# Kernel tuning notes

Measured on AMD Instinct MI355X. Metric: run time of the kernel, lower is better.

Reference implementation:

```python
import jax, jax.numpy as jnp
import numpy as np
from functools import partial

# CUBA LIF/LI constants (from init_kwargs / hxtorch CUBALIFParams defaults)
DT = 1e-6
TAU_MEM = 8e-6
TAU_SYN = 8e-6
DV = DT / TAU_MEM  # 0.125 membrane integration factor
DI = DT / TAU_SYN  # 0.125 synaptic decay factor
ALPHA = 50.0       # SuperSpike surrogate sharpness
THRESHOLD = 1.0    # spike threshold (leak = reset = 0)


@partial(jax.custom_vjp, nondiff_argnums=(1,))
def superspike(x, alpha):
    # Heaviside forward, SuperSpike surrogate backward
    return (x > 0.0).astype(x.dtype)

def _ss_fwd(x, alpha):
    return superspike(x, alpha), x

def _ss_bwd(alpha, x, g):
    return (g / (alpha * jnp.abs(x) + 1.0) ** 2,)

superspike.defvjp(_ss_fwd, _ss_bwd)


def setup_inputs() -> dict:
    key = jax.random.key(0)
    k1, k2, k3 = jax.random.split(key, 3)
    T, B, N_IN, N_H, N_OUT = 512, 128, 256, 1024, 32
    # Bernoulli(0.1) input spike trains (0/1 floats)
    spikes = (jax.random.uniform(k1, (T, B, N_IN)) < 0.1).astype(jnp.float32)
    w_h = jax.random.normal(k2, (N_H, N_IN), jnp.float32) * 0.1
    w_o = jax.random.normal(k3, (N_OUT, N_H), jnp.float32) * 0.05
    return {"spikes": spikes, "w_h": w_h, "w_o": w_o}


def _lif_scan(c):
    # c: [T, B, H] synaptic input currents; returns spike trace z: [T, B, H]
    B, H = c.shape[1], c.shape[2]
    def step(carry, c_t):
        v, i = carry
        i = i * (1.0 - DI) + c_t                 # synaptic current decay + input
        v = v + DV * (i - v)                      # membrane leaky integration (leak=0)
        z = superspike(v - THRESHOLD, ALPHA)      # spike
        zd = jax.lax.stop_gradient(z)
        v = (1.0 - zd) * v                        # reset to 0 (detached spike)
        return (v, i), z
    init = (jnp.zeros((B, H), c.dtype), jnp.zeros((B, H), c.dtype))
    _, z = jax.lax.scan(step, init, c)
    return z


def _li_scan(c):
    # c: [T, B, O]; returns membrane trace v: [T, B, O] (no spike/reset)
    B, O = c.shape[1], c.shape[2]
    def step(carry, c_t):
        v, i = carry
        i = i * (1.0 - DI) + c_t
        v = v + DV * (i - v)
        return (v, i), v
    init = (jnp.zeros((B, O), c.dtype), jnp.zeros((B, O), c.dtype))
    _, v = jax.lax.scan(step, init, c)
    return v


def reference(spikes, w_h, w_o):
    # hidden synapse: dense projection for all timesteps at once
    c_h = jnp.einsum('tbi,hi->tbh', spikes, w_h)
    # hidden CUBA LIF layer (sequential recurrence over time)
    z_h = _lif_scan(c_h)
    # output synapse
    c_o = jnp.einsum('tbh,oh->tbo', z_h, w_o)
    # readout CUBA LI layer -> membrane trace [T, B, n_out]
    return _li_scan(c_o)
```

## Files before the change

kernel.cpp:

```cpp
#include <hip/hip_runtime.h>
#include <stdint.h>

#define T_STEPS 512
#define BATCH   128
#define N_IN    256
#define N_H     1024
#define N_OUT   32

typedef __attribute__((ext_vector_type(2))) float f32x2;


__global__ __launch_bounds__(256) void k_prep(const float* __restrict__ spikes,
                                              uint32_t* __restrict__ pm,
                                              uint16_t* __restrict__ pt,
                                              uint32_t* __restrict__ cnts) {
    __shared__ uint16_t list[64];
    __shared__ uint32_t wcnt[4];
    const int tid = threadIdx.x;
    const int wave = tid >> 6, lane = tid & 63;
    for (int r = 0; r < 4; ++r) {
        const int row = blockIdx.x * 4 + r;
        float s = spikes[(size_t)row * N_IN + tid];
        bool act = s > 0.5f;
        unsigned long long m = __ballot(act);
        if (tid < 64) list[tid] = 256;
        if (lane == 0) wcnt[wave] = (uint32_t)__popcll(m);
        __syncthreads();
        uint32_t off = 0;
        for (int w = 0; w < wave; ++w) off += wcnt[w];
        uint32_t total = wcnt[0] + wcnt[1] + wcnt[2] + wcnt[3];
        if (act) {
            uint32_t pos = off + (uint32_t)__popcll(m & ((1ull << lane) - 1ull));
            if (pos < 64) list[pos] = (uint16_t)tid;
        }
        __syncthreads();
        if (tid < 32) {
            int h = tid >> 4, sl = tid & 15;
            pm[(uint32_t)row * 32 + tid] = ((uint32_t)list[2 * sl + h]) << 8;
        } else if (tid < 64) {
            int u = tid & 31;
            int h = u >> 4, sl = u & 15;
            pt[(uint32_t)row * 32 + u] = list[32 + 2 * sl + h];
        }
        if (tid == 0) cnts[row] = total < 64u ? total : 64u;
        __syncthreads();
    }
}

__global__ __launch_bounds__(256) void k_tr(const float* __restrict__ w_h,
                                            float* __restrict__ w_t) {
    int gid = blockIdx.x * 256 + threadIdx.x;
    int h = gid >> 8, i = gid & 255;
    w_t[(size_t)i * N_H + h] = w_h[gid];
}

__device__ __forceinline__ float xadd32(float x) {
    float a = x, b = x;
    asm("v_permlane32_swap_b32 %0, %1" : "+v"(a), "+v"(b));
    return a + b;
}

struct IdxSet { uint4 a, b, c, d; };

__global__ __launch_bounds__(256) void k_lif(const uint32_t* __restrict__ pm,
                                             const uint16_t* __restrict__ pt,
                                             const uint32_t* __restrict__ cnts,
                                             const float* __restrict__ w_t,
                                             uint32_t* __restrict__ zmask) {
    extern __shared__ __align__(16) float wl[];
    const int bg = blockIdx.x >> 4, tile = blockIdx.x & 15;
    const int h0 = tile * 64, tid = threadIdx.x;

    #pragma unroll 8
    for (int k = 0; k < 16; ++k) {
        int idx = (k << 8) + tid;
        int i = idx >> 4, c4 = (idx & 15) << 2;
        *(float4*)(wl + i * 64 + c4) =
            *(const float4*)(w_t + (size_t)i * N_H + h0 + c4);
    }
    if (tid < 64) wl[256 * 64 + tid] = 0.0f;
    __syncthreads();

    const int wv = __builtin_amdgcn_readfirstlane(tid >> 6);
    const int b  = (bg << 2) + wv;
    const int l  = tid & 63;
    const int duo2 = (l & 31) << 1;
    const int half16 = (l >> 5) << 4;
    const int half32 = (l >> 5) << 4;
    const char* wlb = (const char*)wl + (duo2 << 2);

    int vzero;
    asm("v_mov_b32 %0, 0" : "=v"(vzero));

    uint32_t cW0, cW1, cW2, cW3;
    IdxSet W0, W1, W2, W3;

#define LOADSET(CN, S, ROW) { \
    uint32_t ro_ = (uint32_t)(ROW); \
    CN = *(cnts + ro_ + vzero); \
    const uint4* mp_ = (const uint4*)(pm + ro_ * 32u + half32); \
    S.a = mp_[0]; S.b = mp_[1]; S.c = mp_[2]; S.d = mp_[3]; }

#define GCHUNK4(G, Q) { \
    G += *(const f32x2*)(wlb + (Q).x); \
    G += *(const f32x2*)(wlb + (Q).y); \
    G += *(const f32x2*)(wlb + (Q).z); \
    G += *(const f32x2*)(wlb + (Q).w); }

#define GATHER_MAIN(G, S) { \
    GCHUNK4(G, S.a) GCHUNK4(G, S.b) GCHUNK4(G, S.c) GCHUNK4(G, S.d) }

#define GTCHUNK(G, U0, U1) { \
    uint32_t ia0 = (U0) & 0xFFFFu; \
    uint32_t ia1 = (U0) >> 16; \
    uint32_t ia2 = (U1) & 0xFFFFu; \
    uint32_t ia3 = (U1) >> 16; \
    G += *(const f32x2*)(wl + ia0 * 64 + duo2); \
    G += *(const f32x2*)(wl + ia1 * 64 + duo2); \
    G += *(const f32x2*)(wl + ia2 * 64 + duo2); \
    G += *(const f32x2*)(wl + ia3 * 64 + duo2); }

#define GATHER_TAIL(G, CN, ROW) do { \
    uint32_t cs = __builtin_amdgcn_readfirstlane(CN); \
    if (cs > 32u) { \
        uint32_t ro_ = (uint32_t)(ROW); \
        const uint4* tp = (const uint4*)(pt + ro_ * 32u + half16); \
        uint4 T0 = tp[0], T1 = tp[1]; \
        GTCHUNK(G, T0.x, T0.y) \
        if (cs > 40u) GTCHUNK(G, T0.z, T0.w) \
        if (cs > 48u) GTCHUNK(G, T1.x, T1.y) \
        if (cs > 56u) GTCHUNK(G, T1.z, T1.w) \
    } } while (0)

#define SCANSTEP(G, ROW) { \
    float c0 = xadd32(G.x); \
    float c1 = xadd32(G.y); \
    s0 = __builtin_fmaf(s0, 0.875f, c0); \
    s1 = __builtin_fmaf(s1, 0.875f, c1); \
    v0 = __builtin_fmaf(0.125f, s0 - v0, v0); \
    v1 = __builtin_fmaf(0.125f, s1 - v1, v1); \
    unsigned long long m0 = __ballot(v0 > 1.0f); \
    unsigned long long m1 = __ballot(v1 > 1.0f); \
    if (v0 > 1.0f) v0 = 0.0f; \
    if (v1 > 1.0f) v1 = 0.0f; \
    if (l == 0) { \
        uint2* zp = (uint2*)(zmask + (uint32_t)((ROW) * 32 + (tile << 1))); \
        *zp = make_uint2((uint32_t)m0, (uint32_t)m1); } }

    float v0 = 0, v1 = 0, s0 = 0, s1 = 0;
    LOADSET(cW0, W0, b);
    LOADSET(cW1, W1, BATCH + b);
    LOADSET(cW2, W2, 2 * BATCH + b);
    LOADSET(cW3, W3, 3 * BATCH + b);

    for (int t = 0; t < T_STEPS; t += 4) {
        const int rowA = t * BATCH + b;
        const int rowB = rowA + BATCH;
        const int rowC = rowB + BATCH;
        const int rowD = rowC + BATCH;

        f32x2 ga = {0.0f, 0.0f}, gb = {0.0f, 0.0f};
        GATHER_MAIN(ga, W0);
        GATHER_MAIN(gb, W1);
        GATHER_TAIL(ga, cW0, rowA);
        GATHER_TAIL(gb, cW1, rowB);
        {
            int r4 = t + 4; if (r4 > T_STEPS - 1) r4 = T_STEPS - 1;
            int r5 = t + 5; if (r5 > T_STEPS - 1) r5 = T_STEPS - 1;
            LOADSET(cW0, W0, r4 * BATCH + b);
            LOADSET(cW1, W1, r5 * BATCH + b);
        }
        SCANSTEP(ga, rowA);
        SCANSTEP(gb, rowB);

        f32x2 gc = {0.0f, 0.0f}, gd = {0.0f, 0.0f};
        GATHER_MAIN(gc, W2);
        GATHER_MAIN(gd, W3);
        GATHER_TAIL(gc, cW2, rowC);
        GATHER_TAIL(gd, cW3, rowD);
        {
            int r6 = t + 6; if (r6 > T_STEPS - 1) r6 = T_STEPS - 1;
            int r7 = t + 7; if (r7 > T_STEPS - 1) r7 = T_STEPS - 1;
            LOADSET(cW2, W2, r6 * BATCH + b);
            LOADSET(cW3, W3, r7 * BATCH + b);
        }
        SCANSTEP(gc, rowC);
        SCANSTEP(gd, rowD);
    }
#undef LOADSET
#undef GCHUNK4
#undef GATHER_MAIN
#undef GTCHUNK
#undef GATHER_TAIL
#undef SCANSTEP
}

#define DPP_TERM(X, CTRL) \
    __int_as_float(__builtin_amdgcn_update_dpp(0, __float_as_int(X), CTRL, 0xF, 0xF, true))

__global__ __launch_bounds__(256) void k_li(const uint32_t* __restrict__ zmask,
                                            const float* __restrict__ w_o,
                                            float* __restrict__ out,
                                            float2* __restrict__ svbuf) {
    extern __shared__ __align__(16) float wo[];
    const int gb  = blockIdx.x;
    const int seg = gb >> 10;
    const int rem = gb & 1023;
    const int b   = rem >> 3;
    const int o0  = (rem & 7) << 2;
    const int tid = threadIdx.x;
    for (int lin = tid; lin < 4 * 1024; lin += 256) {
        int ol = lin >> 10, idx = lin & 1023;
        int word = idx >> 5, j = idx & 31;
        int h = ((word >> 1) << 6) + (j << 1) + (word & 1);
        wo[ol * 1056 + word * 33 + j] = w_o[(size_t)(o0 + ol) * N_H + h];
    }
    __syncthreads();

    const int wave = tid >> 6;
    const int word = tid & 31, hsh = ((tid >> 5) & 1) << 4;
    const float* wrow = wo + wave * 1056 + word * 33 + hsh;
    const int t0 = seg << 7, t1 = t0 + 128;

    float v = 0.0f, s = 0.0f;
    uint32_t mA = zmask[(size_t)(t0 * BATCH + b) * 32 + word];
    uint32_t mB = zmask[(size_t)((t0 + 1) * BATCH + b) * 32 + word];
    for (int t = t0; t < t1; t += 2) {
        uint32_t ma = (mA >> hsh) & 0xFFFFu;
        uint32_t mb = (mB >> hsh) & 0xFFFFu;
        int ta = (t + 2 < t1) ? t + 2 : t;
        int tb = (t + 3 < t1) ? t + 3 : t;
        mA = zmask[(size_t)(ta * BATCH + b) * 32 + word];
        mB = zmask[(size_t)(tb * BATCH + b) * 32 + word];

        float c0 = 0.0f, c1 = 0.0f;
        while (ma) { int j = __builtin_ctz(ma); ma &= ma - 1; c0 += wrow[j]; }
        while (mb) { int j = __builtin_ctz(mb); mb &= mb - 1; c1 += wrow[j]; }

        c0 = xadd32(c0);            c1 = xadd32(c1);
        c0 += DPP_TERM(c0, 0x111);  c1 += DPP_TERM(c1, 0x111);
        c0 += DPP_TERM(c0, 0x112);  c1 += DPP_TERM(c1, 0x112);
        c0 += DPP_TERM(c0, 0x114);  c1 += DPP_TERM(c1, 0x114);
        c0 += DPP_TERM(c0, 0x118);  c1 += DPP_TERM(c1, 0x118);
        c0 += DPP_TERM(c0, 0x142);  c1 += DPP_TERM(c1, 0x142);

        s = __builtin_fmaf(s, 0.875f, c0);
        v = __builtin_fmaf(0.125f, s - v, v);
        if ((tid & 63) == 31)
            out[(size_t)(t * BATCH + b) * 32 + o0 + wave] = v;

        s = __builtin_fmaf(s, 0.875f, c1);
        v = __builtin_fmaf(0.125f, s - v, v);
        if ((tid & 63) == 31)
            out[(size_t)((t + 1) * BATCH + b) * 32 + o0 + wave] = v;
    }
    if ((tid & 63) == 31)
        svbuf[((size_t)seg * BATCH + b) * 32 + o0 + wave] = make_float2(s, v);
}

__global__ __launch_bounds__(256) void k_fix(const float2* __restrict__ svbuf,
                                             float* __restrict__ out) {
    int idx = blockIdx.x * 256 + threadIdx.x;
    int o = idx & 31;
    int r = idx >> 5;
    int b = r & 127;
    int t = 128 + (r >> 7);
    int seg = t >> 7;
    int k = (t & 127) + 1;
    const float A128 = 3.7714379e-8f;
    const float C128 = 6.0343007e-7f;
    float2 S = svbuf[(size_t)b * 32 + o];
    if (seg >= 2) {
        float2 z = svbuf[((size_t)BATCH + b) * 32 + o];
        S = make_float2(z.x + A128 * S.x, z.y + A128 * S.y + C128 * S.x);
    }
    if (seg >= 3) {
        float2 z = svbuf[((size_t)2 * BATCH + b) * 32 + o];
        S = make_float2(z.x + A128 * S.x, z.y + A128 * S.y + C128 * S.x);
    }
    float ak = exp2f((float)k * -0.19264508f);
    float corr = __builtin_fmaf(ak, S.y, 0.125f * (float)k * ak * S.x);
    out[(size_t)(t * BATCH + b) * 32 + o] += corr;
}

extern "C" void kernel_launch(void* const* d_in, const int* in_sizes, int n_in,
                              void* d_out, int out_size, void* d_ws, size_t ws_size,
                              hipStream_t stream) {
    const float* spikes = (const float*)d_in[0];
    const float* w_h    = (const float*)d_in[1];
    const float* w_o    = (const float*)d_in[2];
    float* out = (float*)d_out;

    char* ws = (char*)d_ws;
    uint32_t* pm    = (uint32_t*)(ws);
    uint16_t* pt    = (uint16_t*)(ws + 8388608);
    uint32_t* cnts  = (uint32_t*)(ws + 12582912);
    float*    w_t   = (float*)   (ws + 12845056);
    uint32_t* zmask = (uint32_t*)(ws + 13893632);
    float2*   svbuf = (float2*)  (ws);

    const int lds12 = (256 * 64 + 64) * 4;
    const int lds34 = 4 * 1056 * 4;
    hipFuncSetAttribute((const void*)k_lif, hipFuncAttributeMaxDynamicSharedMemorySize, lds12);
    hipFuncSetAttribute((const void*)k_li,  hipFuncAttributeMaxDynamicSharedMemorySize, lds34);

    k_prep<<<(T_STEPS * BATCH) / 4, 256, 0, stream>>>(spikes, pm, pt, cnts);
    k_tr<<<(N_H * N_IN) / 256, 256, 0, stream>>>(w_h, w_t);
    k_lif<<<512, 256, lds12, stream>>>(pm, pt, cnts, w_t, zmask);
    k_li<<<4 * BATCH * 8, 256, lds34, stream>>>(zmask, w_o, out, svbuf);
    k_fix<<<(384 * BATCH * N_OUT) / 256, 256, 0, stream>>>(svbuf, out);
}
```

Measured before the change: 456.0 us.

## Restructure LI readout to gather float4 weights per spike across outputs

The LI readout kernel now stores four output channels interleaved in LDS, so each set spike bit does a single float4 load instead of separate scalar loads for each output wave. Each wave handles one batch row, with the two half-waves processing two timesteps that are exchanged via permlane32 swap. This cuts the grid by 4x and reduces the per-spike mask decode work. The trade-off is that each thread now walks a full 32-bit mask rather than 16 bits, which lengthens the serial inner loop and lowers parallelism.

```diff
diff --git a/kernel.cpp b/kernel.cpp
--- a/kernel.cpp
+++ b/kernel.cpp
@@ -60,6 +60,12 @@
     return a + b;
 }
 
+__device__ __forceinline__ float xpick(float x) {
+    float a = x, b = x;
+    asm("v_permlane32_swap_b32 %0, %1" : "+v"(a), "+v"(b));
+    return (a != x) ? a : b;
+}
+
 struct IdxSet { uint4 a, b, c, d; };
 
 __global__ __launch_bounds__(256) void k_lif(const uint32_t* __restrict__ pm,
@@ -202,60 +208,82 @@
                                             const float* __restrict__ w_o,
                                             float* __restrict__ out,
                                             float2* __restrict__ svbuf) {
-    extern __shared__ __align__(16) float wo[];
+    extern __shared__ __align__(16) float wo4[];
     const int gb  = blockIdx.x;
-    const int seg = gb >> 10;
-    const int rem = gb & 1023;
-    const int b   = rem >> 3;
-    const int o0  = (rem & 7) << 2;
+    const int seg = gb >> 8;
+    const int rem = gb & 255;
+    const int bq  = rem >> 3;
+    const int oct = rem & 7;
+    const int o0  = oct << 2;
     const int tid = threadIdx.x;
-    for (int lin = tid; lin < 4 * 1024; lin += 256) {
-        int ol = lin >> 10, idx = lin & 1023;
-        int word = idx >> 5, j = idx & 31;
-        int h = ((word >> 1) << 6) + (j << 1) + (word & 1);
-        wo[ol * 1056 + word * 33 + j] = w_o[(size_t)(o0 + ol) * N_H + h];
+
+    for (int lin = tid; lin < 4096; lin += 256) {
+        int o = lin & 3, idx = lin >> 2;
+        int h = ((idx >> 6) << 6) + ((idx & 31) << 1) + ((idx >> 5) & 1);
+        wo4[((idx + (idx >> 3)) << 2) + o] = w_o[(size_t)(o0 + o) * N_H + h];
     }
     __syncthreads();
 
-    const int wave = tid >> 6;
-    const int word = tid & 31, hsh = ((tid >> 5) & 1) << 4;
-    const float* wrow = wo + wave * 1056 + word * 33 + hsh;
+    const int b    = (bq << 2) + (tid >> 6);
+    const int l    = tid & 63;
+    const int word = l & 31;
+    const int tofs = l >> 5;
+    const uint32_t baseoff = (uint32_t)(576 * word);
+    const char* wbase = (const char*)wo4 + baseoff;
     const int t0 = seg << 7, t1 = t0 + 128;
 
-    float v = 0.0f, s = 0.0f;
-    uint32_t mA = zmask[(size_t)(t0 * BATCH + b) * 32 + word];
-    uint32_t mB = zmask[(size_t)((t0 + 1) * BATCH + b) * 32 + word];
+    float s0 = 0, s1 = 0, s2 = 0, s3 = 0;
+    float v0 = 0, v1 = 0, v2 = 0, v3 = 0;
+
+    uint32_t mcur = zmask[(uint32_t)((t0 + tofs) * BATCH + b) * 32 + word];
     for (int t = t0; t < t1; t += 2) {
-        uint32_t ma = (mA >> hsh) & 0xFFFFu;
-        uint32_t mb = (mB >> hsh) & 0xFFFFu;
-        int ta = (t + 2 < t1) ? t + 2 : t;
-        int tb = (t + 3 < t1) ? t + 3 : t;
-        mA = zmask[(size_t)(ta * BATCH + b) * 32 + word];
-        mB = zmask[(size_t)(tb * BATCH + b) * 32 + word];
-
-        float c0 = 0.0f, c1 = 0.0f;
-        while (ma) { int j = __builtin_ctz(ma); ma &= ma - 1; c0 += wrow[j]; }
-        while (mb) { int j = __builtin_ctz(mb); mb &= mb - 1; c1 += wrow[j]; }
-
-        c0 = xadd32(c0);            c1 = xadd32(c1);
-        c0 += DPP_TERM(c0, 0x111);  c1 += DPP_TERM(c1, 0x111);
-        c0 += DPP_TERM(c0, 0x112);  c1 += DPP_TERM(c1, 0x112);
-        c0 += DPP_TERM(c0, 0x114);  c1 += DPP_TERM(c1, 0x114);
-        c0 += DPP_TERM(c0, 0x118);  c1 += DPP_TERM(c1, 0x118);
-        c0 += DPP_TERM(c0, 0x142);  c1 += DPP_TERM(c1, 0x142);
-
-        s = __builtin_fmaf(s, 0.875f, c0);
-        v = __builtin_fmaf(0.125f, s - v, v);
-        if ((tid & 63) == 31)
-            out[(size_t)(t * BATCH + b) * 32 + o0 + wave] = v;
-
-        s = __builtin_fmaf(s, 0.875f, c1);
-        v = __builtin_fmaf(0.125f, s - v, v);
-        if ((tid & 63) == 31)
-            out[(size_t)((t + 1) * BATCH + b) * 32 + o0 + wave] = v;
-    }
-    if ((tid & 63) == 31)
-        svbuf[((size_t)seg * BATCH + b) * 32 + o0 + wave] = make_float2(s, v);
+        uint32_t ma = mcur;
+        int tp = t + 2; if (tp >= t1) tp = t0;
+        mcur = zmask[(uint32_t)((tp + tofs) * BATCH + b) * 32 + word];
+
+        float a0 = 0.0f, a1 = 0.0f, a2 = 0.0f, a3 = 0.0f;
+        while (ma) {
+            int j = __builtin_ctz(ma); ma &= ma - 1;
+            const float4 wv = *(const float4*)(wbase + (((j + (j >> 3)) << 4)));
+            a0 += wv.x; a1 += wv.y; a2 += wv.z; a3 += wv.w;
+        }
+
+        a0 += DPP_TERM(a0, 0x111); a1 += DPP_TERM(a1, 0x111);
+        a2 += DPP_TERM(a2, 0x111); a3 += DPP_TERM(a3, 0x111);
+        a0 += DPP_TERM(a0, 0x112); a1 += DPP_TERM(a1, 0x112);
+        a2 += DPP_TERM(a2, 0x112); a3 += DPP_TERM(a3, 0x112);
+        a0 += DPP_TERM(a0, 0x114); a1 += DPP_TERM(a1, 0x114);
+        a2 += DPP_TERM(a2, 0x114); a3 += DPP_TERM(a3, 0x114);
+        a0 += DPP_TERM(a0, 0x118); a1 += DPP_TERM(a1, 0x118);
+        a2 += DPP_TERM(a2, 0x118); a3 += DPP_TERM(a3, 0x118);
+        a0 += DPP_TERM(a0, 0x142); a1 += DPP_TERM(a1, 0x142);
+        a2 += DPP_TERM(a2, 0x142); a3 += DPP_TERM(a3, 0x142);
+
+        float b0 = xpick(a0), b1 = xpick(a1), b2 = xpick(a2), b3 = xpick(a3);
+
+        s0 = __builtin_fmaf(s0, 0.875f, a0); v0 = __builtin_fmaf(0.125f, s0 - v0, v0);
+        s1 = __builtin_fmaf(s1, 0.875f, a1); v1 = __builtin_fmaf(0.125f, s1 - v1, v1);
+        s2 = __builtin_fmaf(s2, 0.875f, a2); v2 = __builtin_fmaf(0.125f, s2 - v2, v2);
+        s3 = __builtin_fmaf(s3, 0.875f, a3); v3 = __builtin_fmaf(0.125f, s3 - v3, v3);
+        if (l == 31)
+            *(float4*)(out + (size_t)(t * BATCH + b) * 32 + o0) =
+                make_float4(v0, v1, v2, v3);
+
+        s0 = __builtin_fmaf(s0, 0.875f, b0); v0 = __builtin_fmaf(0.125f, s0 - v0, v0);
+        s1 = __builtin_fmaf(s1, 0.875f, b1); v1 = __builtin_fmaf(0.125f, s1 - v1, v1);
+        s2 = __builtin_fmaf(s2, 0.875f, b2); v2 = __builtin_fmaf(0.125f, s2 - v2, v2);
+        s3 = __builtin_fmaf(s3, 0.875f, b3); v3 = __builtin_fmaf(0.125f, s3 - v3, v3);
+        if (l == 31)
+            *(float4*)(out + (size_t)((t + 1) * BATCH + b) * 32 + o0) =
+                make_float4(v0, v1, v2, v3);
+    }
+    if (l == 31) {
+        float2* sp = svbuf + ((size_t)seg * BATCH + b) * 32 + o0;
+        sp[0] = make_float2(s0, v0);
+        sp[1] = make_float2(s1, v1);
+        sp[2] = make_float2(s2, v2);
+        sp[3] = make_float2(s3, v3);
+    }
 }
 
 __global__ __launch_bounds__(256) void k_fix(const float2* __restrict__ svbuf,
@@ -300,13 +328,13 @@
     float2*   svbuf = (float2*)  (ws);
 
     const int lds12 = (256 * 64 + 64) * 4;
-    const int lds34 = 4 * 1056 * 4;
+    const int lds34 = 1152 * 16;
     hipFuncSetAttribute((const void*)k_lif, hipFuncAttributeMaxDynamicSharedMemorySize, lds12);
     hipFuncSetAttribute((const void*)k_li,  hipFuncAttributeMaxDynamicSharedMemorySize, lds34);
 
     k_prep<<<(T_STEPS * BATCH) / 4, 256, 0, stream>>>(spikes, pm, pt, cnts);
     k_tr<<<(N_H * N_IN) / 256, 256, 0, stream>>>(w_h, w_t);
     k_lif<<<512, 256, lds12, stream>>>(pm, pt, cnts, w_t, zmask);
-    k_li<<<4 * BATCH * 8, 256, lds34, stream>>>(zmask, w_o, out, svbuf);
+    k_li<<<4 * 32 * 8, 256, lds34, stream>>>(zmask, w_o, out, svbuf);
     k_fix<<<(384 * BATCH * N_OUT) / 256, 256, 0, stream>>>(svbuf, out);
 }
```

Result: faster. 400.9 us (-12.1%).
